# Performance work log

Measured on AMD Instinct MI355X. Metric: run time of the kernel, lower is better.

## Reference

```python
import jax, jax.numpy as jnp
import numpy as np

N = 100000      # num nodes
E = 1600000     # num edges
D_IN = 128
D_OUT = 64
PRELU_INIT = 0.25


def setup_inputs() -> dict:
    key = jax.random.key(0)
    k1, k2, k3, k4, k5 = jax.random.split(key, 5)
    node_x = jax.random.normal(k1, (N, D_IN), dtype=jnp.float32)
    edge_rows = jax.random.randint(k2, (E,), 0, N, dtype=jnp.int32)
    edge_cols = jax.random.randint(k3, (E,), 0, N, dtype=jnp.int32)
    edge_vals = jax.random.uniform(k4, (E,), dtype=jnp.float32)
    # Xavier-uniform init for weights
    limit = float(np.sqrt(6.0 / (D_IN + D_OUT)))
    weights = jax.random.uniform(k5, (D_IN, D_OUT), dtype=jnp.float32,
                                 minval=-limit, maxval=limit)
    prelu_a = jnp.float32(PRELU_INIT)
    return {"node_x": node_x, "edge_rows": edge_rows, "edge_cols": edge_cols,
            "edge_vals": edge_vals, "weights": weights, "prelu_a": prelu_a}


def reference(node_x, edge_rows, edge_cols, edge_vals, weights, prelu_a):
    # Dense projection: [N, D_IN] @ [D_IN, D_OUT] -> [N, D_OUT]
    support = jnp.matmul(node_x, weights)
    # Sparse-dense matmul: output[r] = sum_{(r,c,v) in adj} v * support[c]
    messages = edge_vals[:, None] * support[edge_cols]  # [E, D_OUT]
    output = jax.ops.segment_sum(messages, edge_rows, num_segments=N)
    # PReLU with single learned scalar
    out = jnp.where(output > 0, output, prelu_a * output)
    return (out, support)
```

## Files before the change

### kernel.cpp

```cpp
#include <hip/hip_runtime.h>

#define N_NODES 100000
#define N_EDGES 1600000
#define D_IN    128
#define D_OUT   64

#define XT_STRIDE 260
#define NBUCKETS 1563
#define NBW 782
#define G 392
#define SLICE 4096
#define M_FLAT (NBUCKETS * G)
#define SCANA_BLOCKS 599
typedef unsigned long long ull;
typedef unsigned int uint;

__global__ __launch_bounds__(256) void gcn_gemm(
    const float* __restrict__ x,
    const float* __restrict__ w,
    float* __restrict__ support)
{
    __shared__ float wl[D_IN * D_OUT];
    __shared__ float xT[32 * XT_STRIDE];

    const int t  = threadIdx.x;
    const int tx = t & 7;
    const int ty = t >> 3;
    const long row0 = (long)blockIdx.x * 256;

    {
        const float4* wf  = (const float4*)w;
        float4*       wlf = (float4*)wl;
#pragma unroll
        for (int j = 0; j < 8; ++j)
            wlf[t + 256 * j] = wf[t + 256 * j];
    }

    float acc[8][8];
#pragma unroll
    for (int i = 0; i < 8; ++i)
#pragma unroll
        for (int j = 0; j < 8; ++j)
            acc[i][j] = 0.f;

    for (int kc = 0; kc < 4; ++kc) {
        const int k0 = kc * 32;
        __syncthreads();

        const int kk = tx * 4;
#pragma unroll
        for (int it = 0; it < 8; ++it) {
            const int  rg   = it * 32 + ty;
            const long grow = row0 + rg;
            float4 v = make_float4(0.f, 0.f, 0.f, 0.f);
            if (grow < N_NODES)
                v = *(const float4*)&x[grow * D_IN + k0 + kk];
            xT[(kk + 0) * XT_STRIDE + rg] = v.x;
            xT[(kk + 1) * XT_STRIDE + rg] = v.y;
            xT[(kk + 2) * XT_STRIDE + rg] = v.z;
            xT[(kk + 3) * XT_STRIDE + rg] = v.w;
        }
        __syncthreads();

#pragma unroll 8
        for (int k = 0; k < 32; ++k) {
            const float4 a0 = *(const float4*)&xT[k * XT_STRIDE + ty * 8];
            const float4 a1 = *(const float4*)&xT[k * XT_STRIDE + ty * 8 + 4];
            const float4 b0 = *(const float4*)&wl[(k0 + k) * D_OUT + tx * 8];
            const float4 b1 = *(const float4*)&wl[(k0 + k) * D_OUT + tx * 8 + 4];
            const float av[8] = {a0.x, a0.y, a0.z, a0.w, a1.x, a1.y, a1.z, a1.w};
            const float bv[8] = {b0.x, b0.y, b0.z, b0.w, b1.x, b1.y, b1.z, b1.w};
#pragma unroll
            for (int i = 0; i < 8; ++i)
#pragma unroll
                for (int j = 0; j < 8; ++j)
                    acc[i][j] = fmaf(av[i], bv[j], acc[i][j]);
        }
    }

#pragma unroll
    for (int i = 0; i < 8; ++i) {
        const long r = row0 + ty * 8 + i;
        if (r < N_NODES) {
            float4 o0 = make_float4(acc[i][0], acc[i][1], acc[i][2], acc[i][3]);
            float4 o1 = make_float4(acc[i][4], acc[i][5], acc[i][6], acc[i][7]);
            *(float4*)&support[r * D_OUT + tx * 8]     = o0;
            *(float4*)&support[r * D_OUT + tx * 8 + 4] = o1;
        }
    }
}

__global__ __launch_bounds__(256) void k_cnt(
    const int* __restrict__ rows, uint* __restrict__ S)
{
    __shared__ uint hist[NBW];
    const int t = threadIdx.x;
    const int b = (blockIdx.x & 7) * 49 + (blockIdx.x >> 3);
    for (int i = t; i < NBW; i += 256) hist[i] = 0u;
    __syncthreads();

    const int base = b * SLICE;
#pragma unroll 4
    for (int s2 = 0; s2 < 16; ++s2) {
        const int e = base + s2 * 256 + t;
        if (e < N_EDGES) {
            const uint bk = (uint)rows[e] >> 6;
            atomicAdd(&hist[bk >> 1], 1u << ((bk & 1) * 16));
        }
    }
    __syncthreads();

    for (int i = t; i < NBUCKETS; i += 256)
        S[(size_t)i * G + b] = (hist[i >> 1] >> ((i & 1) * 16)) & 0xffffu;
}

__global__ __launch_bounds__(256) void k_scanA(
    uint* __restrict__ S, uint* __restrict__ bsum)
{
    __shared__ uint s[256];
    const int t = threadIdx.x;
    const size_t base = (size_t)blockIdx.x * 1024 + (size_t)t * 4;
    uint4 v = make_uint4(0u, 0u, 0u, 0u);
    if (base < M_FLAT) v = *(const uint4*)&S[base];
    const uint tsum = v.x + v.y + v.z + v.w;
    s[t] = tsum;
    __syncthreads();
#pragma unroll
    for (int off = 1; off < 256; off <<= 1) {
        const uint add = (t >= off) ? s[t - off] : 0u;
        __syncthreads();
        s[t] += add;
        __syncthreads();
    }
    const uint eb = s[t] - tsum;
    if (t == 255) bsum[blockIdx.x] = s[255];
    if (base < M_FLAT) {
        uint4 o;
        o.x = eb; o.y = eb + v.x; o.z = o.y + v.y; o.w = o.z + v.z;
        *(uint4*)&S[base] = o;
    }
}

__global__ __launch_bounds__(1024) void k_scanB(uint* __restrict__ bsum)
{
    __shared__ uint s[1024];
    const int t = threadIdx.x;
    const uint v = (t < SCANA_BLOCKS) ? bsum[t] : 0u;
    s[t] = v;
    __syncthreads();
#pragma unroll
    for (int off = 1; off < 1024; off <<= 1) {
        const uint add = (t >= off) ? s[t - off] : 0u;
        __syncthreads();
        s[t] += add;
        __syncthreads();
    }
    if (t < SCANA_BLOCKS) bsum[t] = s[t] - v;
}

__global__ __launch_bounds__(256) void k_scanC(
    uint* __restrict__ S, const uint* __restrict__ bsum)
{
    const uint add = bsum[blockIdx.x];
    const size_t base = (size_t)blockIdx.x * 1024 + (size_t)threadIdx.x * 4;
    if (base < M_FLAT) {
        uint4 v = *(const uint4*)&S[base];
        v.x += add; v.y += add; v.z += add; v.w += add;
        *(uint4*)&S[base] = v;
    }
}

__global__ __launch_bounds__(256) void k_scatter(
    const int* __restrict__ rows, const int* __restrict__ cols,
    const float* __restrict__ vals, const uint* __restrict__ S,
    ull* __restrict__ pairs)
{
    __shared__ uint cur[NBUCKETS];
    const int t = threadIdx.x;
    const int b = (blockIdx.x & 7) * 49 + (blockIdx.x >> 3);
    for (int i = t; i < NBUCKETS; i += 256) cur[i] = S[(size_t)i * G + b];
    __syncthreads();

    const int base = b * SLICE;
#pragma unroll 4
    for (int s2 = 0; s2 < 16; ++s2) {
        const int e = base + s2 * 256 + t;
        if (e < N_EDGES) {
            const uint r  = (uint)rows[e];
            const uint bk = r >> 6;
            const uint rl = r & 63u;
            const uint pos = atomicAdd(&cur[bk], 1u);
            pairs[pos] = ((ull)__float_as_uint(vals[e]) << 32)
                       | (rl << 17) | (uint)cols[e];
        }
    }
}

__global__ __launch_bounds__(256) void k_bsort(
    const uint* __restrict__ S, const ull* __restrict__ pairs,
    ull* __restrict__ pairs2, int* __restrict__ offsets,
    int* __restrict__ counts)
{
    __shared__ uint h[64], ex[64], cur[64];
    const int k = blockIdx.x;
    const int t = threadIdx.x;
    const int beg = (int)S[(size_t)k * G];
    const int end = (k == NBUCKETS - 1) ? N_EDGES : (int)S[(size_t)(k + 1) * G];

    if (t < 64) h[t] = 0u;
    __syncthreads();

    for (int i = beg + t; i < end; i += 256)
        atomicAdd(&h[((uint)pairs[i] >> 17) & 63u], 1u);
    __syncthreads();

    if (t < 64) ex[t] = h[t];
    __syncthreads();
#pragma unroll
    for (int off = 1; off < 64; off <<= 1) {
        const uint add = (t >= off && t < 64) ? ex[t - off] : 0u;
        __syncthreads();
        if (t < 64) ex[t] += add;
        __syncthreads();
    }
    if (t < 64) {
        const uint e0 = ex[t] - h[t];
        cur[t] = (uint)beg + e0;
        const int row = k * 64 + t;
        if (row < N_NODES) {
            counts[row]  = (int)h[t];
            offsets[row] = beg + (int)e0;
        }
    }
    __syncthreads();

    for (int i = beg + t; i < end; i += 256) {
        const ull p = pairs[i];
        const uint rl = ((uint)p >> 17) & 63u;
        const uint pos = atomicAdd(&cur[rl], 1u);
        pairs2[pos] = p;
    }
}

__global__ __launch_bounds__(256) void k_rowsum(
    const int* __restrict__ offsets, const int* __restrict__ counts,
    const ull* __restrict__ pairs, const float* __restrict__ support,
    const float* __restrict__ prelu_a, float* __restrict__ out)
{
    const int lane = threadIdx.x & 63;
    const int row  = blockIdx.x * 4 + (threadIdx.x >> 6);

    const int start = offsets[row];
    const int deg   = counts[row];

    float acc = 0.f;
    int j = 0;
    for (; j + 8 <= deg; j += 8) {
        ull p[8];
#pragma unroll
        for (int u = 0; u < 8; ++u) p[u] = pairs[start + j + u];
        float s[8];
#pragma unroll
        for (int u = 0; u < 8; ++u)
            s[u] = support[(size_t)((uint)p[u] & 0x1ffffu) * D_OUT + lane];
#pragma unroll
        for (int u = 0; u < 8; ++u)
            acc = fmaf(__uint_as_float((uint)(p[u] >> 32)), s[u], acc);
    }
    for (; j + 4 <= deg; j += 4) {
        ull p[4];
#pragma unroll
        for (int u = 0; u < 4; ++u) p[u] = pairs[start + j + u];
        float s[4];
#pragma unroll
        for (int u = 0; u < 4; ++u)
            s[u] = support[(size_t)((uint)p[u] & 0x1ffffu) * D_OUT + lane];
#pragma unroll
        for (int u = 0; u < 4; ++u)
            acc = fmaf(__uint_as_float((uint)(p[u] >> 32)), s[u], acc);
    }
    for (; j < deg; ++j) {
        const ull p = pairs[start + j];
        const float s = support[(size_t)((uint)p & 0x1ffffu) * D_OUT + lane];
        acc = fmaf(__uint_as_float((uint)(p >> 32)), s, acc);
    }

    const float a = prelu_a[0];
    out[(size_t)row * D_OUT + lane] = acc > 0.f ? acc : a * acc;
}

extern "C" void kernel_launch(void* const* d_in, const int* in_sizes, int n_in,
                              void* d_out, int out_size, void* d_ws, size_t ws_size,
                              hipStream_t stream) {
    const float* x    = (const float*)d_in[0];
    const int*   rows = (const int*)d_in[1];
    const int*   cols = (const int*)d_in[2];
    const float* vals = (const float*)d_in[3];
    const float* w    = (const float*)d_in[4];
    const float* pa   = (const float*)d_in[5];

    float* out     = (float*)d_out;
    float* support = out + (size_t)N_NODES * D_OUT;

    uint* S       = (uint*)d_ws;
    uint* bsumA   = S + (size_t)SCANA_BLOCKS * 1024;
    int*  offsets = (int*)(bsumA + 1024);
    int*  counts  = offsets + 100032;
    ull*  pairs   = (ull*)(counts + 100032);
    ull*  pairs2  = pairs + N_EDGES;

    gcn_gemm <<<(N_NODES + 255) / 256, 256, 0, stream>>>(x, w, support);
    k_cnt    <<<G, 256, 0, stream>>>(rows, S);
    k_scanA  <<<SCANA_BLOCKS, 256, 0, stream>>>(S, bsumA);
    k_scanB  <<<1, 1024, 0, stream>>>(bsumA);
    k_scanC  <<<SCANA_BLOCKS, 256, 0, stream>>>(S, bsumA);
    k_scatter<<<G, 256, 0, stream>>>(rows, cols, vals, S, pairs);
    k_bsort  <<<NBUCKETS, 256, 0, stream>>>(S, pairs, pairs2, offsets, counts);
    k_rowsum <<<N_NODES / 4, 256, 0, stream>>>(offsets, counts, pairs2, support, pa, out);
}
```

Measured before the change: 264.9 us.

## Fuse GEMM with histogram, fold scan fixup, merge bucket sort with row SpMM

Runs the edge histogram blocks in the same launch as the dense GEMM, folds the scan's block-offset add into the scatter and bucket kernels, and replaces the global bucket sort plus row-sum kernels with one kernel that sorts each bucket in shared memory and computes the row sums directly. This removes three launches and a full round trip of the pairs array through global memory. In exchange the bucket kernel uses 32KB of LDS, which lowers occupancy. Buckets larger than CAP fall back to a slow quadratic path.

```diff
diff --git a/kernel.cpp b/kernel.cpp
--- a/kernel.cpp
+++ b/kernel.cpp
@@ -12,18 +12,46 @@
 #define SLICE 4096
 #define M_FLAT (NBUCKETS * G)
 #define SCANA_BLOCKS 599
+#define GEMM_BLOCKS 391
+#define CAP 2048
 typedef unsigned long long ull;
 typedef unsigned int uint;
 
-__global__ __launch_bounds__(256) void gcn_gemm(
+__global__ __launch_bounds__(256) void k_gemm_cnt(
     const float* __restrict__ x,
     const float* __restrict__ w,
-    float* __restrict__ support)
+    float* __restrict__ support,
+    const int* __restrict__ rows,
+    uint* __restrict__ S)
 {
     __shared__ float wl[D_IN * D_OUT];
     __shared__ float xT[32 * XT_STRIDE];
 
-    const int t  = threadIdx.x;
+    const int t = threadIdx.x;
+
+    if (blockIdx.x >= GEMM_BLOCKS) {
+        uint* hist = (uint*)wl;
+        const int bid = blockIdx.x - GEMM_BLOCKS;
+        const int b = (bid & 7) * 49 + (bid >> 3);
+        for (int i = t; i < NBW; i += 256) hist[i] = 0u;
+        __syncthreads();
+
+        const int base = b * SLICE;
+#pragma unroll 4
+        for (int s2 = 0; s2 < 16; ++s2) {
+            const int e = base + s2 * 256 + t;
+            if (e < N_EDGES) {
+                const uint bk = (uint)rows[e] >> 6;
+                atomicAdd(&hist[bk >> 1], 1u << ((bk & 1) * 16));
+            }
+        }
+        __syncthreads();
+
+        for (int i = t; i < NBUCKETS; i += 256)
+            S[(size_t)i * G + b] = (hist[i >> 1] >> ((i & 1) * 16)) & 0xffffu;
+        return;
+    }
+
     const int tx = t & 7;
     const int ty = t >> 3;
     const long row0 = (long)blockIdx.x * 256;
@@ -90,30 +118,6 @@
     }
 }
 
-__global__ __launch_bounds__(256) void k_cnt(
-    const int* __restrict__ rows, uint* __restrict__ S)
-{
-    __shared__ uint hist[NBW];
-    const int t = threadIdx.x;
-    const int b = (blockIdx.x & 7) * 49 + (blockIdx.x >> 3);
-    for (int i = t; i < NBW; i += 256) hist[i] = 0u;
-    __syncthreads();
-
-    const int base = b * SLICE;
-#pragma unroll 4
-    for (int s2 = 0; s2 < 16; ++s2) {
-        const int e = base + s2 * 256 + t;
-        if (e < N_EDGES) {
-            const uint bk = (uint)rows[e] >> 6;
-            atomicAdd(&hist[bk >> 1], 1u << ((bk & 1) * 16));
-        }
-    }
-    __syncthreads();
-
-    for (int i = t; i < NBUCKETS; i += 256)
-        S[(size_t)i * G + b] = (hist[i >> 1] >> ((i & 1) * 16)) & 0xffffu;
-}
-
 __global__ __launch_bounds__(256) void k_scanA(
     uint* __restrict__ S, uint* __restrict__ bsum)
 {
@@ -158,27 +162,22 @@
     if (t < SCANA_BLOCKS) bsum[t] = s[t] - v;
 }
 
-__global__ __launch_bounds__(256) void k_scanC(
-    uint* __restrict__ S, const uint* __restrict__ bsum)
-{
-    const uint add = bsum[blockIdx.x];
-    const size_t base = (size_t)blockIdx.x * 1024 + (size_t)threadIdx.x * 4;
-    if (base < M_FLAT) {
-        uint4 v = *(const uint4*)&S[base];
-        v.x += add; v.y += add; v.z += add; v.w += add;
-        *(uint4*)&S[base] = v;
-    }
-}
-
 __global__ __launch_bounds__(256) void k_scatter(
     const int* __restrict__ rows, const int* __restrict__ cols,
     const float* __restrict__ vals, const uint* __restrict__ S,
-    ull* __restrict__ pairs)
+    const uint* __restrict__ bsum, ull* __restrict__ pairs)
 {
     __shared__ uint cur[NBUCKETS];
+    __shared__ uint bs[SCANA_BLOCKS + 1];
     const int t = threadIdx.x;
     const int b = (blockIdx.x & 7) * 49 + (blockIdx.x >> 3);
-    for (int i = t; i < NBUCKETS; i += 256) cur[i] = S[(size_t)i * G + b];
+
+    for (int i = t; i < SCANA_BLOCKS; i += 256) bs[i] = bsum[i];
+    __syncthreads();
+    for (int i = t; i < NBUCKETS; i += 256) {
+        const size_t f = (size_t)i * G + b;
+        cur[i] = S[f] + bs[f >> 10];
+    }
     __syncthreads();
 
     const int base = b * SLICE;
@@ -196,97 +195,117 @@
     }
 }
 
-__global__ __launch_bounds__(256) void k_bsort(
-    const uint* __restrict__ S, const ull* __restrict__ pairs,
-    ull* __restrict__ pairs2, int* __restrict__ offsets,
-    int* __restrict__ counts)
-{
-    __shared__ uint h[64], ex[64], cur[64];
-    const int k = blockIdx.x;
-    const int t = threadIdx.x;
-    const int beg = (int)S[(size_t)k * G];
-    const int end = (k == NBUCKETS - 1) ? N_EDGES : (int)S[(size_t)(k + 1) * G];
-
-    if (t < 64) h[t] = 0u;
-    __syncthreads();
-
-    for (int i = beg + t; i < end; i += 256)
-        atomicAdd(&h[((uint)pairs[i] >> 17) & 63u], 1u);
-    __syncthreads();
-
-    if (t < 64) ex[t] = h[t];
-    __syncthreads();
-#pragma unroll
-    for (int off = 1; off < 64; off <<= 1) {
-        const uint add = (t >= off && t < 64) ? ex[t - off] : 0u;
-        __syncthreads();
-        if (t < 64) ex[t] += add;
-        __syncthreads();
-    }
-    if (t < 64) {
-        const uint e0 = ex[t] - h[t];
-        cur[t] = (uint)beg + e0;
-        const int row = k * 64 + t;
-        if (row < N_NODES) {
-            counts[row]  = (int)h[t];
-            offsets[row] = beg + (int)e0;
-        }
-    }
-    __syncthreads();
-
-    for (int i = beg + t; i < end; i += 256) {
-        const ull p = pairs[i];
-        const uint rl = ((uint)p >> 17) & 63u;
-        const uint pos = atomicAdd(&cur[rl], 1u);
-        pairs2[pos] = p;
-    }
-}
-
-__global__ __launch_bounds__(256) void k_rowsum(
-    const int* __restrict__ offsets, const int* __restrict__ counts,
+__global__ __launch_bounds__(256) void k_bucket(
+    const uint* __restrict__ S, const uint* __restrict__ bsum,
     const ull* __restrict__ pairs, const float* __restrict__ support,
     const float* __restrict__ prelu_a, float* __restrict__ out)
 {
-    const int lane = threadIdx.x & 63;
-    const int row  = blockIdx.x * 4 + (threadIdx.x >> 6);
-
-    const int start = offsets[row];
-    const int deg   = counts[row];
-
-    float acc = 0.f;
-    int j = 0;
-    for (; j + 8 <= deg; j += 8) {
-        ull p[8];
-#pragma unroll
-        for (int u = 0; u < 8; ++u) p[u] = pairs[start + j + u];
-        float s[8];
-#pragma unroll
-        for (int u = 0; u < 8; ++u)
-            s[u] = support[(size_t)((uint)p[u] & 0x1ffffu) * D_OUT + lane];
-#pragma unroll
-        for (int u = 0; u < 8; ++u)
-            acc = fmaf(__uint_as_float((uint)(p[u] >> 32)), s[u], acc);
-    }
-    for (; j + 4 <= deg; j += 4) {
-        ull p[4];
-#pragma unroll
-        for (int u = 0; u < 4; ++u) p[u] = pairs[start + j + u];
-        float s[4];
-#pragma unroll
-        for (int u = 0; u < 4; ++u)
-            s[u] = support[(size_t)((uint)p[u] & 0x1ffffu) * D_OUT + lane];
-#pragma unroll
-        for (int u = 0; u < 4; ++u)
-            acc = fmaf(__uint_as_float((uint)(p[u] >> 32)), s[u], acc);
-    }
-    for (; j < deg; ++j) {
-        const ull p = pairs[start + j];
-        const float s = support[(size_t)((uint)p & 0x1ffffu) * D_OUT + lane];
-        acc = fmaf(__uint_as_float((uint)(p >> 32)), s, acc);
-    }
-
+    __shared__ ull seg[CAP];
+    __shared__ ull srt[CAP];
+    __shared__ uint h[64], ex[64], rowoff[64], cur[64];
+    const int k = blockIdx.x;
+    const int t = threadIdx.x, w = t >> 6, lane = t & 63;
+
+    const size_t f0 = (size_t)k * G;
+    const int beg = (int)(S[f0] + bsum[f0 >> 10]);
+    int end;
+    if (k == NBUCKETS - 1) end = N_EDGES;
+    else {
+        const size_t f1 = f0 + G;
+        end = (int)(S[f1] + bsum[f1 >> 10]);
+    }
+    const int n = end - beg;
     const float a = prelu_a[0];
-    out[(size_t)row * D_OUT + lane] = acc > 0.f ? acc : a * acc;
+
+    if (t < 64) h[t] = 0u;
+    __syncthreads();
+
+    if (n <= CAP) {
+        for (int i = t; i < n; i += 256) {
+            const ull p = pairs[beg + i];
+            seg[i] = p;
+            atomicAdd(&h[((uint)p >> 17) & 63u], 1u);
+        }
+        __syncthreads();
+
+        if (t < 64) ex[t] = h[t];
+        __syncthreads();
+#pragma unroll
+        for (int off = 1; off < 64; off <<= 1) {
+            const uint add = (t >= off && t < 64) ? ex[t - off] : 0u;
+            __syncthreads();
+            if (t < 64) ex[t] += add;
+            __syncthreads();
+        }
+        if (t < 64) {
+            rowoff[t] = ex[t] - h[t];
+            cur[t]    = rowoff[t];
+        }
+        __syncthreads();
+
+        for (int i = t; i < n; i += 256) {
+            const ull p = seg[i];
+            const uint pos = atomicAdd(&cur[((uint)p >> 17) & 63u], 1u);
+            srt[pos] = p;
+        }
+        __syncthreads();
+
+        for (int q = 0; q < 16; ++q) {
+            const int rl  = w * 16 + q;
+            const long row = (long)k * 64 + rl;
+            if (row >= N_NODES) break;
+            const int st  = (int)rowoff[rl];
+            const int deg = (int)h[rl];
+
+            float acc = 0.f;
+            int j = 0;
+            for (; j + 8 <= deg; j += 8) {
+                ull p[8];
+#pragma unroll
+                for (int u = 0; u < 8; ++u) p[u] = srt[st + j + u];
+                float sv[8];
+#pragma unroll
+                for (int u = 0; u < 8; ++u)
+                    sv[u] = support[(size_t)((uint)p[u] & 0x1ffffu) * D_OUT + lane];
+#pragma unroll
+                for (int u = 0; u < 8; ++u)
+                    acc = fmaf(__uint_as_float((uint)(p[u] >> 32)), sv[u], acc);
+            }
+            for (; j + 4 <= deg; j += 4) {
+                ull p[4];
+#pragma unroll
+                for (int u = 0; u < 4; ++u) p[u] = srt[st + j + u];
+                float sv[4];
+#pragma unroll
+                for (int u = 0; u < 4; ++u)
+                    sv[u] = support[(size_t)((uint)p[u] & 0x1ffffu) * D_OUT + lane];
+#pragma unroll
+                for (int u = 0; u < 4; ++u)
+                    acc = fmaf(__uint_as_float((uint)(p[u] >> 32)), sv[u], acc);
+            }
+            for (; j < deg; ++j) {
+                const ull p = srt[st + j];
+                acc = fmaf(__uint_as_float((uint)(p >> 32)),
+                           support[(size_t)((uint)p & 0x1ffffu) * D_OUT + lane], acc);
+            }
+            out[row * D_OUT + lane] = acc > 0.f ? acc : a * acc;
+        }
+    } else {
+        for (int q = 0; q < 16; ++q) {
+            const int rl  = w * 16 + q;
+            const long row = (long)k * 64 + rl;
+            if (row >= N_NODES) break;
+            float acc = 0.f;
+            for (int i = 0; i < n; ++i) {
+                const ull p = pairs[beg + i];
+                if ((((uint)p >> 17) & 63u) == (uint)rl)
+                    acc = fmaf(__uint_as_float((uint)(p >> 32)),
+                               support[(size_t)((uint)p & 0x1ffffu) * D_OUT + lane],
+                               acc);
+            }
+            out[row * D_OUT + lane] = acc > 0.f ? acc : a * acc;
+        }
+    }
 }
 
 extern "C" void kernel_launch(void* const* d_in, const int* in_sizes, int n_in,
@@ -302,19 +321,13 @@
     float* out     = (float*)d_out;
     float* support = out + (size_t)N_NODES * D_OUT;
 
-    uint* S       = (uint*)d_ws;
-    uint* bsumA   = S + (size_t)SCANA_BLOCKS * 1024;
-    int*  offsets = (int*)(bsumA + 1024);
-    int*  counts  = offsets + 100032;
-    ull*  pairs   = (ull*)(counts + 100032);
-    ull*  pairs2  = pairs + N_EDGES;
-
-    gcn_gemm <<<(N_NODES + 255) / 256, 256, 0, stream>>>(x, w, support);
-    k_cnt    <<<G, 256, 0, stream>>>(rows, S);
-    k_scanA  <<<SCANA_BLOCKS, 256, 0, stream>>>(S, bsumA);
-    k_scanB  <<<1, 1024, 0, stream>>>(bsumA);
-    k_scanC  <<<SCANA_BLOCKS, 256, 0, stream>>>(S, bsumA);
-    k_scatter<<<G, 256, 0, stream>>>(rows, cols, vals, S, pairs);
-    k_bsort  <<<NBUCKETS, 256, 0, stream>>>(S, pairs, pairs2, offsets, counts);
-    k_rowsum <<<N_NODES / 4, 256, 0, stream>>>(offsets, counts, pairs2, support, pa, out);
-}
+    uint* S     = (uint*)d_ws;
+    uint* bsum  = S + (size_t)SCANA_BLOCKS * 1024;
+    ull*  pairs = (ull*)(bsum + 1024);
+
+    k_gemm_cnt<<<GEMM_BLOCKS + G, 256, 0, stream>>>(x, w, support, rows, S);
+    k_scanA   <<<SCANA_BLOCKS, 256, 0, stream>>>(S, bsum);
+    k_scanB   <<<1, 1024, 0, stream>>>(bsum);
+    k_scatter <<<G, 256, 0, stream>>>(rows, cols, vals, S, bsum, pairs);
+    k_bucket  <<<NBUCKETS, 256, 0, stream>>>(S, bsum, pairs, support, pa, out);
+}
```

After: 251.5 us. 1.05x faster.
